# Optimization experiments

Measured on AMD Instinct MI355X. Metric: run time of the kernel, lower is better.

The kernel has to match this reference:

```python
import jax, jax.numpy as jnp
import numpy as np

CODEBOOK_SIZE = 8192
TEMP = 1.0  # sample_codebook_temp


def l2norm(t, eps=1e-12):
    # matches F.normalize(t, p=2, dim=-1)
    n = jnp.sqrt(jnp.sum(t * t, axis=-1, keepdims=True))
    return t / jnp.maximum(n, eps)


def setup_inputs() -> dict:
    key = jax.random.key(0)
    kx, ke = jax.random.split(key)
    x = jax.random.normal(kx, (1, 16, 1024, 512), dtype=jnp.float32)
    # learned codebook, stored l2-normalized as in uniform_init -> l2norm
    embed = l2norm(jax.random.normal(ke, (1, 8192, 512), dtype=jnp.float32))
    return {"x": x, "embed": embed}


def reference(x, embed):
    # x: [h, b, n, d]  embed: [h, c, d]
    h, d = x.shape[0], x.shape[-1]
    shape = x.shape
    flatten = l2norm(x.reshape(h, -1, d))          # transform_input = l2norm, pack 'h * d'
    embed_n = l2norm(embed)                        # cosine-sim codebook
    # cosine similarity logits: [h, N, c]
    dist = jnp.einsum('hnd,hcd->hnc', flatten, embed_n)
    # gumbel_sample with stochastic=False: plain argmax of logits
    embed_ind = jnp.argmax(dist, axis=-1)          # [h, N]
    one_hot = jax.nn.one_hot(embed_ind, CODEBOOK_SIZE, dtype=dist.dtype)
    # straight-through (learnable codebook, training): hard + soft - sg(soft)
    soft = jax.nn.softmax(dist / TEMP, axis=-1)
    one_hot_st = one_hot + soft - jax.lax.stop_gradient(soft)
    # quantize via one-hot mix of codebook vectors: [h, N, d]
    quantize = jnp.einsum('hnc,hcd->hnd', one_hot_st, embed_n)
    quantize = quantize.reshape(shape)
    embed_ind = embed_ind.reshape(shape[:-1])
    return quantize, embed_ind, dist
```

## Files before the change

### kernel.cpp

```cpp
#include <hip/hip_runtime.h>
#include <math.h>

#define N_ROWS 16384
#define C_CODES 8192
#define DIM 512
#define I_OFS (N_ROWS * DIM)
#define D_OFS (I_OFS + N_ROWS)

typedef __bf16 bf16;
typedef bf16 bf16x8 __attribute__((ext_vector_type(8)));
typedef float f32x4 __attribute__((ext_vector_type(4)));

__device__ __forceinline__ void gload16(void* lds, const void* g) {
  __builtin_amdgcn_global_load_lds((__attribute__((address_space(1))) void*)(g),
                                   (__attribute__((address_space(3))) void*)(lds), 16, 0, 0);
}

__global__ void norm_embed(const float* __restrict__ embed, float* __restrict__ en,
                           bf16* __restrict__ enb) {
  int wave = threadIdx.x >> 6, lane = threadIdx.x & 63;
  int row = blockIdx.x * 4 + wave;
  const float* src = embed + (size_t)row * DIM;
  float4 v0 = ((const float4*)src)[lane * 2];
  float4 v1 = ((const float4*)src)[lane * 2 + 1];
  float s = v0.x * v0.x + v0.y * v0.y + v0.z * v0.z + v0.w * v0.w +
            v1.x * v1.x + v1.y * v1.y + v1.z * v1.z + v1.w * v1.w;
  for (int m = 1; m < 64; m <<= 1) s += __shfl_xor(s, m, 64);
  float nrm = fmaxf(sqrtf(s), 1e-12f);
  float4 o0, o1;
  o0.x = v0.x / nrm; o0.y = v0.y / nrm; o0.z = v0.z / nrm; o0.w = v0.w / nrm;
  o1.x = v1.x / nrm; o1.y = v1.y / nrm; o1.z = v1.z / nrm; o1.w = v1.w / nrm;
  float* dst = en + (size_t)row * DIM;
  ((float4*)dst)[lane * 2] = o0;
  ((float4*)dst)[lane * 2 + 1] = o1;
  bf16x8 b;
  b[0] = (bf16)o0.x; b[1] = (bf16)o0.y; b[2] = (bf16)o0.z; b[3] = (bf16)o0.w;
  b[4] = (bf16)o1.x; b[5] = (bf16)o1.y; b[6] = (bf16)o1.z; b[7] = (bf16)o1.w;
  *(bf16x8*)(enb + (size_t)row * DIM + lane * 8) = b;
}

__global__ void norm_x(const float* __restrict__ x, bf16* __restrict__ xnb,
                       float* __restrict__ xnorm) {
  int wave = threadIdx.x >> 6, lane = threadIdx.x & 63;
  int row = blockIdx.x * 4 + wave;
  const float* src = x + (size_t)row * DIM;
  float4 v0 = ((const float4*)src)[lane * 2];
  float4 v1 = ((const float4*)src)[lane * 2 + 1];
  float s = v0.x * v0.x + v0.y * v0.y + v0.z * v0.z + v0.w * v0.w +
            v1.x * v1.x + v1.y * v1.y + v1.z * v1.z + v1.w * v1.w;
  for (int m = 1; m < 64; m <<= 1) s += __shfl_xor(s, m, 64);
  float nrm = fmaxf(sqrtf(s), 1e-12f);
  if (lane == 0) xnorm[row] = nrm;
  bf16x8 b;
  b[0] = (bf16)(v0.x / nrm); b[1] = (bf16)(v0.y / nrm);
  b[2] = (bf16)(v0.z / nrm); b[3] = (bf16)(v0.w / nrm);
  b[4] = (bf16)(v1.x / nrm); b[5] = (bf16)(v1.y / nrm);
  b[6] = (bf16)(v1.z / nrm); b[7] = (bf16)(v1.w / nrm);
  *(bf16x8*)(xnb + (size_t)row * DIM + lane * 8) = b;
}

#define BM 128
#define BN 128
#define BK 32

__global__ __launch_bounds__(256, 2) void gemm_dist(
    const bf16* __restrict__ xnb, const bf16* __restrict__ enb,
    float* __restrict__ dist, float* __restrict__ tilemax) {
  __shared__ bf16 As[BM * BK];
  __shared__ bf16 Bs[BN * BK];
  __shared__ float wmax[2][128];

  int tid = threadIdx.x;
  int cb = blockIdx.x;
  int rb = blockIdx.y;
  int rowBase = rb * BM, colBase = cb * BN;
  int wave = tid >> 6, lane = tid & 63;
  int wr = wave >> 1, wc = wave & 1;
  int row16 = lane & 15, quad = lane >> 4;

  f32x4 acc[4][4];
  f32x4 zero = {0.f, 0.f, 0.f, 0.f};
  for (int i = 0; i < 4; ++i)
    for (int j = 0; j < 4; ++j) acc[i][j] = zero;

  int e0 = tid * 8;
  int e1 = 2048 + tid * 8;
  int m0 = e0 >> 5, k0 = e0 & 31;
  int m1 = e1 >> 5, k1 = e1 & 31;
  const bf16* ga0 = xnb + (size_t)(rowBase + m0) * DIM + k0;
  const bf16* ga1 = xnb + (size_t)(rowBase + m1) * DIM + k1;
  const bf16* gb0 = enb + (size_t)(colBase + m0) * DIM + k0;
  const bf16* gb1 = enb + (size_t)(colBase + m1) * DIM + k1;

  for (int kt = 0; kt < DIM / BK; ++kt) {
    int ko = kt * BK;
    gload16(&As[e0], ga0 + ko);
    gload16(&As[e1], ga1 + ko);
    gload16(&Bs[e0], gb0 + ko);
    gload16(&Bs[e1], gb1 + ko);
    __syncthreads();
    bf16x8 a[4], b[4];
    for (int i = 0; i < 4; ++i)
      a[i] = *(const bf16x8*)&As[(wr * 64 + i * 16 + row16) * BK + quad * 8];
    for (int j = 0; j < 4; ++j)
      b[j] = *(const bf16x8*)&Bs[(wc * 64 + j * 16 + row16) * BK + quad * 8];
    for (int i = 0; i < 4; ++i)
      for (int j = 0; j < 4; ++j)
        acc[i][j] = __builtin_amdgcn_mfma_f32_16x16x32_bf16(a[i], b[j], acc[i][j], 0, 0, 0);
    __syncthreads();
  }

  for (int i = 0; i < 4; ++i) {
    int gr = rowBase + wr * 64 + i * 16 + quad * 4;
    for (int j = 0; j < 4; ++j) {
      int gc = colBase + wc * 64 + j * 16 + row16;
      for (int r = 0; r < 4; ++r)
        dist[(size_t)(gr + r) * C_CODES + gc] = acc[i][j][r];
    }
  }

  for (int i = 0; i < 4; ++i) {
    float rm[4];
    for (int r = 0; r < 4; ++r)
      rm[r] = fmaxf(fmaxf(acc[i][0][r], acc[i][1][r]), fmaxf(acc[i][2][r], acc[i][3][r]));
    for (int m = 1; m < 16; m <<= 1)
      for (int r = 0; r < 4; ++r) rm[r] = fmaxf(rm[r], __shfl_xor(rm[r], m, 64));
    if (row16 == 0)
      for (int r = 0; r < 4; ++r) wmax[wc][wr * 64 + i * 16 + quad * 4 + r] = rm[r];
  }
  __syncthreads();
  if (tid < 128) {
    float m = fmaxf(wmax[0][tid], wmax[1][tid]);
    tilemax[(size_t)(rowBase + tid) * 64 + cb] = m;
  }
}

#define EPS 0.01f
#define MAXC 32

__global__ void refine(const float* __restrict__ x, const float* __restrict__ en,
                       const float* __restrict__ xnorm, const float* __restrict__ tilemax,
                       const float* __restrict__ dist, float* __restrict__ out) {
  int r = blockIdx.x, t = threadIdx.x;
  __shared__ float tm[64];
  __shared__ float red[256];
  __shared__ int cand[MAXC];
  __shared__ float cdot[MAXC];
  __shared__ int ncand;
  __shared__ int bestIdx;

  if (t == 0) ncand = 0;
  if (t < 64) tm[t] = tilemax[(size_t)r * 64 + t];
  __syncthreads();
  red[t] = (t < 64) ? tm[t] : -3.0e38f;
  __syncthreads();
  for (int s = 128; s > 0; s >>= 1) {
    if (t < s) red[t] = fmaxf(red[t], red[t + s]);
    __syncthreads();
  }
  float T = red[0] - EPS;
  __syncthreads();

  const float* drow = dist + (size_t)r * C_CODES;
  for (int cbB = 0; cbB < 64; ++cbB) {
    if (tm[cbB] >= T && t < 128) {
      int col = cbB * 128 + t;
      float v = drow[col];
      if (v >= T) {
        int p = atomicAdd(&ncand, 1);
        if (p < MAXC) cand[p] = col;
      }
    }
  }
  __syncthreads();
  int nc = min(ncand, MAXC);

  const float* xr = x + (size_t)r * DIM;
  float nrm = xnorm[r];
  for (int k = 0; k < nc; ++k) {
    const float* er = en + (size_t)cand[k] * DIM;
    red[t] = xr[t] * er[t] + xr[t + 256] * er[t + 256];
    __syncthreads();
    for (int s = 128; s > 0; s >>= 1) {
      if (t < s) red[t] += red[t + s];
      __syncthreads();
    }
    if (t == 0) cdot[k] = red[0] / nrm;
    __syncthreads();
  }

  if (t == 0) {
    float bv = -3.0e38f;
    int bi = 0x7fffffff;
    for (int k = 0; k < nc; ++k) {
      float v = cdot[k];
      int c = cand[k];
      if (v > bv || (v == bv && c < bi)) { bv = v; bi = c; }
    }
    bestIdx = bi;
    out[I_OFS + r] = (float)bi;
  }
  __syncthreads();
  int bi = bestIdx;
  const float* eb = en + (size_t)bi * DIM;
  out[(size_t)r * DIM + t] = eb[t];
  out[(size_t)r * DIM + t + 256] = eb[t + 256];
}

extern "C" void kernel_launch(void* const* d_in, const int* in_sizes, int n_in,
                              void* d_out, int out_size, void* d_ws, size_t ws_size,
                              hipStream_t stream) {
  const float* x = (const float*)d_in[0];
  const float* embed = (const float*)d_in[1];
  float* out = (float*)d_out;
  char* ws = (char*)d_ws;
  bf16* enb = (bf16*)(ws);
  bf16* xnb = (bf16*)(ws + 8388608);
  float* en = (float*)(ws + 25165824);
  float* xnorm = (float*)(ws + 41943040);
  float* tilemax = (float*)(ws + 42008576);

  hipLaunchKernelGGL(norm_embed, dim3(C_CODES / 4), dim3(256), 0, stream, embed, en, enb);
  hipLaunchKernelGGL(norm_x, dim3(N_ROWS / 4), dim3(256), 0, stream, x, xnb, xnorm);
  hipLaunchKernelGGL(gemm_dist, dim3(C_CODES / BN, N_ROWS / BM), dim3(256), 0, stream,
                     xnb, enb, out + D_OFS, tilemax);
  hipLaunchKernelGGL(refine, dim3(N_ROWS), dim3(256), 0, stream,
                     x, en, xnorm, tilemax, out + D_OFS, out);
}
```

Before: 785.9 us.

## Rewrite refine as one wave per row with ballot-based candidate scan

```diff
diff --git a/kernel.cpp b/kernel.cpp
--- a/kernel.cpp
+++ b/kernel.cpp
@@ -136,75 +136,64 @@
 }
 
 #define EPS 0.01f
-#define MAXC 32
-
-__global__ void refine(const float* __restrict__ x, const float* __restrict__ en,
-                       const float* __restrict__ xnorm, const float* __restrict__ tilemax,
-                       const float* __restrict__ dist, float* __restrict__ out) {
-  int r = blockIdx.x, t = threadIdx.x;
-  __shared__ float tm[64];
-  __shared__ float red[256];
-  __shared__ int cand[MAXC];
-  __shared__ float cdot[MAXC];
-  __shared__ int ncand;
-  __shared__ int bestIdx;
-
-  if (t == 0) ncand = 0;
-  if (t < 64) tm[t] = tilemax[(size_t)r * 64 + t];
-  __syncthreads();
-  red[t] = (t < 64) ? tm[t] : -3.0e38f;
-  __syncthreads();
-  for (int s = 128; s > 0; s >>= 1) {
-    if (t < s) red[t] = fmaxf(red[t], red[t + s]);
-    __syncthreads();
-  }
-  float T = red[0] - EPS;
-  __syncthreads();
+
+__global__ __launch_bounds__(256) void refine(
+    const float* __restrict__ x, const float* __restrict__ en,
+    const float* __restrict__ xnorm, const float* __restrict__ tilemax,
+    const float* __restrict__ dist, float* __restrict__ out) {
+  int wave = threadIdx.x >> 6, lane = threadIdx.x & 63;
+  int r = blockIdx.x * 4 + wave;
+
+  float tmv = tilemax[(size_t)r * 64 + lane];
+  float m = tmv;
+#pragma unroll
+  for (int s = 1; s < 64; s <<= 1) m = fmaxf(m, __shfl_xor(m, s, 64));
+  float T = m - EPS;
+
+  const float* xr = x + (size_t)r * DIM;
+  float4 xv0 = ((const float4*)xr)[lane * 2];
+  float4 xv1 = ((const float4*)xr)[lane * 2 + 1];
+  float nrm = xnorm[r];
 
   const float* drow = dist + (size_t)r * C_CODES;
-  for (int cbB = 0; cbB < 64; ++cbB) {
-    if (tm[cbB] >= T && t < 128) {
-      int col = cbB * 128 + t;
-      float v = drow[col];
-      if (v >= T) {
-        int p = atomicAdd(&ncand, 1);
-        if (p < MAXC) cand[p] = col;
+  float bv = -3.0e38f;
+  int bi = 0x7fffffff;
+
+  unsigned long long smask = __ballot(tmv >= T);
+  while (smask) {
+    int cbB = __builtin_ctzll(smask);
+    smask &= smask - 1;
+    int base = cbB * 128;
+    float v0 = drow[base + lane];
+    float v1 = drow[base + 64 + lane];
+    unsigned long long b0 = __ballot(v0 >= T);
+    unsigned long long b1 = __ballot(v1 >= T);
+    while (b0 | b1) {
+      int c;
+      if (b0) {
+        int l = __builtin_ctzll(b0); b0 &= b0 - 1; c = base + l;
+      } else {
+        int l = __builtin_ctzll(b1); b1 &= b1 - 1; c = base + 64 + l;
       }
-    }
-  }
-  __syncthreads();
-  int nc = min(ncand, MAXC);
-
-  const float* xr = x + (size_t)r * DIM;
-  float nrm = xnorm[r];
-  for (int k = 0; k < nc; ++k) {
-    const float* er = en + (size_t)cand[k] * DIM;
-    red[t] = xr[t] * er[t] + xr[t + 256] * er[t + 256];
-    __syncthreads();
-    for (int s = 128; s > 0; s >>= 1) {
-      if (t < s) red[t] += red[t + s];
-      __syncthreads();
-    }
-    if (t == 0) cdot[k] = red[0] / nrm;
-    __syncthreads();
-  }
-
-  if (t == 0) {
-    float bv = -3.0e38f;
-    int bi = 0x7fffffff;
-    for (int k = 0; k < nc; ++k) {
-      float v = cdot[k];
-      int c = cand[k];
+      const float* er = en + (size_t)c * DIM;
+      float4 e0 = ((const float4*)er)[lane * 2];
+      float4 e1 = ((const float4*)er)[lane * 2 + 1];
+      float d = xv0.x * e0.x + xv0.y * e0.y + xv0.z * e0.z + xv0.w * e0.w +
+                xv1.x * e1.x + xv1.y * e1.y + xv1.z * e1.z + xv1.w * e1.w;
+#pragma unroll
+      for (int s = 1; s < 64; s <<= 1) d += __shfl_xor(d, s, 64);
+      float v = d / nrm;
       if (v > bv || (v == bv && c < bi)) { bv = v; bi = c; }
     }
-    bestIdx = bi;
-    out[I_OFS + r] = (float)bi;
-  }
-  __syncthreads();
-  int bi = bestIdx;
+  }
+
+  if (lane == 0) out[I_OFS + r] = (float)bi;
   const float* eb = en + (size_t)bi * DIM;
-  out[(size_t)r * DIM + t] = eb[t];
-  out[(size_t)r * DIM + t + 256] = eb[t + 256];
+  float4 q0 = ((const float4*)eb)[lane * 2];
+  float4 q1 = ((const float4*)eb)[lane * 2 + 1];
+  float* orow = out + (size_t)r * DIM;
+  ((float4*)orow)[lane * 2] = q0;
+  ((float4*)orow)[lane * 2 + 1] = q1;
 }
 
 extern "C" void kernel_launch(void* const* d_in, const int* in_sizes, int n_in,
@@ -224,6 +213,6 @@
   hipLaunchKernelGGL(norm_x, dim3(N_ROWS / 4), dim3(256), 0, stream, x, xnb, xnorm);
   hipLaunchKernelGGL(gemm_dist, dim3(C_CODES / BN, N_ROWS / BM), dim3(256), 0, stream,
                      xnb, enb, out + D_OFS, tilemax);
-  hipLaunchKernelGGL(refine, dim3(N_ROWS), dim3(256), 0, stream,
+  hipLaunchKernelGGL(refine, dim3(N_ROWS / 4), dim3(256), 0, stream,
                      x, en, xnorm, tilemax, out + D_OFS, out);
 }
```

Measured after the change: 739.9 us. -5.9%, faster.
